# Optimization experiments

Measured on AMD Instinct MI355X. Metric: run time of the kernel, lower is better.

Reference implementation:

```python
import jax, jax.numpy as jnp
import numpy as np

N = 100000   # nodes
E = 1600000  # edges (avg degree 16)
D = 64       # channels (in = hidden = out)
L = 3        # layers


def setup_inputs() -> dict:
    key = jax.random.key(0)
    ks = jax.random.split(key, 8)
    s = 1.0 / np.sqrt(D)
    x = jax.random.normal(ks[0], (N, D), jnp.float32)
    edge_index = jax.random.randint(ks[1], (2, E), 0, N, dtype=jnp.int32)
    edge_type = jax.random.randint(ks[2], (E,), 0, 5, dtype=jnp.int32)
    Wq = jax.random.normal(ks[3], (L, D, D), jnp.float32) * s
    Wk = jax.random.normal(ks[4], (L, D, D), jnp.float32) * s
    Wv = jax.random.normal(ks[5], (L, D, D), jnp.float32) * s
    Ws = jax.random.normal(ks[6], (L, D, D), jnp.float32) * s
    bq = jnp.zeros((L, D), jnp.float32)
    bk = jnp.zeros((L, D), jnp.float32)
    bv = jnp.zeros((L, D), jnp.float32)
    bs = jnp.zeros((L, D), jnp.float32)
    return {"x": x, "edge_index": edge_index, "edge_type": edge_type,
            "Wq": Wq, "bq": bq, "Wk": Wk, "bk": bk,
            "Wv": Wv, "bv": bv, "Ws": Ws, "bs": bs}


def _transformer_conv(x, src, dst, Wq, bq, Wk, bk, Wv, bv, Ws, bs):
    # PyG TransformerConv, heads=1, concat=True, root_weight=True, beta=False
    q = x @ Wq + bq            # [N, D]
    k = x @ Wk + bk            # [N, D]
    v = x @ Wv + bv            # [N, D]
    scale = 1.0 / jnp.sqrt(jnp.asarray(D, x.dtype))
    # per-edge attention logits: <q_i, k_j> / sqrt(D)
    alpha = jnp.sum(q[dst] * k[src], axis=-1) * scale   # [E]
    # scatter-softmax over incoming edges of each target node
    m = jax.ops.segment_max(alpha, dst, num_segments=N)  # [N]
    e = jnp.exp(alpha - m[dst])                          # [E]
    denom = jax.ops.segment_sum(e, dst, num_segments=N)  # [N]
    a = e / (denom[dst] + 1e-16)                         # [E]
    # scatter-add aggregation of alpha * v_j
    agg = jax.ops.segment_sum(a[:, None] * v[src], dst, num_segments=N)  # [N, D]
    # root/skip connection (lin_skip with bias)
    return agg + x @ Ws + bs


def reference(x, edge_index, edge_type, Wq, bq, Wk, bk, Wv, bv, Ws, bs):
    src, dst = edge_index[0], edge_index[1]
    h = x
    for i in range(L):
        h = _transformer_conv(h, src, dst, Wq[i], bq[i], Wk[i], bk[i],
                              Wv[i], bv[i], Ws[i], bs[i])
        if i < L - 1:
            h = jax.nn.relu(h)
            # F.dropout(p=0.4) is identity in eval mode
    return h
```

## Files before the change

kernel.cpp:

```cpp
#include <hip/hip_runtime.h>

#define D 64
#define LAYERS 3
#define BSHIFT 8
#define NBMAX 512
#define CHUNK 4096
#define WSTRIDE 72

typedef unsigned short ushort_t;
typedef __bf16 bf16x8 __attribute__((ext_vector_type(8)));
typedef float f32x4 __attribute__((ext_vector_type(4)));

__device__ __forceinline__ ushort_t f2bf(float f) {
    unsigned b = __float_as_uint(f);
    b += 0x7FFFu + ((b >> 16) & 1u);
    return (ushort_t)(b >> 16);
}
__device__ __forceinline__ float bflo(unsigned u) { return __uint_as_float(u << 16); }
__device__ __forceinline__ float bfhi(unsigned u) { return __uint_as_float(u & 0xFFFF0000u); }

__global__ __launch_bounds__(256) void proj_kernel(
    const float* __restrict__ x,
    const float* __restrict__ Wq, const float* __restrict__ bq,
    const float* __restrict__ Wk, const float* __restrict__ bk,
    const float* __restrict__ Wv, const float* __restrict__ bv,
    const float* __restrict__ Ws, const float* __restrict__ bs,
    ushort_t* __restrict__ qb, ushort_t* __restrict__ kv,
    ushort_t* __restrict__ sk, int N)
{
    __shared__ ushort_t xs[32 * WSTRIDE];
    __shared__ ushort_t wt[4 * 64 * WSTRIDE];

    const int t = threadIdx.x;
    const int block_row = blockIdx.x * 32;

    {
        const int r  = t >> 3;
        const int c8 = (t & 7) * 8;
        const int row = block_row + r;
        float4 x0, x1;
        if (row < N) {
            x0 = *(const float4*)(x + (size_t)row * D + c8);
            x1 = *(const float4*)(x + (size_t)row * D + c8 + 4);
        } else {
            x0 = make_float4(0.f,0.f,0.f,0.f); x1 = x0;
        }
        uint4 u;
        u.x = (unsigned)f2bf(x0.x) | ((unsigned)f2bf(x0.y) << 16);
        u.y = (unsigned)f2bf(x0.z) | ((unsigned)f2bf(x0.w) << 16);
        u.z = (unsigned)f2bf(x1.x) | ((unsigned)f2bf(x1.y) << 16);
        u.w = (unsigned)f2bf(x1.z) | ((unsigned)f2bf(x1.w) << 16);
        *(uint4*)(xs + r * WSTRIDE + c8) = u;
    }
    {
        const float* Wm[4] = {Wq, Wk, Wv, Ws};
#pragma unroll
        for (int m = 0; m < 4; ++m) {
            const float* W = Wm[m];
            ushort_t* wtm = wt + m * 64 * WSTRIDE;
#pragma unroll
            for (int i = 0; i < 16; ++i) {
                const int e = i * 256 + t;
                const int k = e >> 6, n = e & 63;
                wtm[n * WSTRIDE + k] = f2bf(W[e]);
            }
        }
    }
    __syncthreads();

    const int l  = t & 63;
    const int w  = t >> 6;
    const int lr = l & 15;
    const int lk = (l >> 4) * 8;

    bf16x8 afr[2][2];
#pragma unroll
    for (int rt = 0; rt < 2; ++rt)
#pragma unroll
        for (int ks = 0; ks < 2; ++ks)
            afr[rt][ks] = *(const bf16x8*)(xs + (rt*16 + lr) * WSTRIDE + ks*32 + lk);

    const ushort_t* wtw = wt + w * 64 * WSTRIDE;
    f32x4 acc[2][4];
#pragma unroll
    for (int rt = 0; rt < 2; ++rt)
#pragma unroll
        for (int ct = 0; ct < 4; ++ct)
            acc[rt][ct] = (f32x4){0.f, 0.f, 0.f, 0.f};

#pragma unroll
    for (int ct = 0; ct < 4; ++ct) {
        const bf16x8 b0 = *(const bf16x8*)(wtw + (ct*16 + lr) * WSTRIDE + lk);
        const bf16x8 b1 = *(const bf16x8*)(wtw + (ct*16 + lr) * WSTRIDE + 32 + lk);
        acc[0][ct] = __builtin_amdgcn_mfma_f32_16x16x32_bf16(afr[0][0], b0, acc[0][ct], 0, 0, 0);
        acc[0][ct] = __builtin_amdgcn_mfma_f32_16x16x32_bf16(afr[0][1], b1, acc[0][ct], 0, 0, 0);
        acc[1][ct] = __builtin_amdgcn_mfma_f32_16x16x32_bf16(afr[1][0], b0, acc[1][ct], 0, 0, 0);
        acc[1][ct] = __builtin_amdgcn_mfma_f32_16x16x32_bf16(afr[1][1], b1, acc[1][ct], 0, 0, 0);
    }

    const float* biasW = (w == 0) ? bq : (w == 1) ? bk : (w == 2) ? bv : bs;
    float bcol[4];
#pragma unroll
    for (int ct = 0; ct < 4; ++ct) bcol[ct] = biasW[ct*16 + lr];

#pragma unroll
    for (int rt = 0; rt < 2; ++rt) {
#pragma unroll
        for (int ct = 0; ct < 4; ++ct) {
#pragma unroll
            for (int r = 0; r < 4; ++r) {
                const int row = block_row + rt*16 + (l >> 4) * 4 + r;
                const int col = ct*16 + lr;
                if (row < N) {
                    const float val = acc[rt][ct][r] + bcol[ct];
                    if (w == 0)      qb[(size_t)row * D + col] = f2bf(val);
                    else if (w == 3) sk[(size_t)row * D + col] = f2bf(val);
                    else {
                        ushort_t* kvr = kv + (size_t)row * 128;
                        kvr[(col >> 2) * 8 + ((w == 2) ? 4 : 0) + (col & 3)] = f2bf(val);
                    }
                }
            }
        }
    }
}

__global__ __launch_bounds__(256) void b_hist_kernel(
    const int* __restrict__ dst, int* __restrict__ bcount, int E)
{
    __shared__ int h[NBMAX];
    const int t = threadIdx.x;
    h[t] = 0; h[t + 256] = 0;
    __syncthreads();
    const int base = blockIdx.x * CHUNK;
#pragma unroll
    for (int i = 0; i < 16; ++i) {
        const int e = base + i * 256 + t;
        if (e < E) atomicAdd(h + (dst[e] >> BSHIFT), 1);
    }
    __syncthreads();
    if (h[t])       atomicAdd(bcount + t, h[t]);
    if (h[t + 256]) atomicAdd(bcount + t + 256, h[t + 256]);
}

__global__ __launch_bounds__(512) void b_scan_kernel(
    const int* __restrict__ bcount, int* __restrict__ bbase,
    int* __restrict__ gcursor, int E)
{
    __shared__ int tmp[NBMAX];
    const int t = threadIdx.x;
    const int val = bcount[t];
    tmp[t] = val;
    __syncthreads();
    for (int off = 1; off < NBMAX; off <<= 1) {
        int x = (t >= off) ? tmp[t - off] : 0;
        __syncthreads();
        tmp[t] += x;
        __syncthreads();
    }
    const int excl = tmp[t] - val;
    bbase[t] = excl;
    gcursor[t] = excl;
    if (t == NBMAX - 1) bbase[NBMAX] = E;
}

__global__ __launch_bounds__(256) void b_scatter_kernel(
    const int* __restrict__ src, const int* __restrict__ dst,
    int* __restrict__ gcursor, uint2* __restrict__ packed, int E)
{
    __shared__ int h[NBMAX];
    __shared__ int gb[NBMAX];
    const int t = threadIdx.x;
    h[t] = 0; h[t + 256] = 0;
    __syncthreads();

    const int base = blockIdx.x * CHUNK;
    int ls[16], ld[16], lr[16];
#pragma unroll
    for (int i = 0; i < 16; ++i) {
        const int e = base + i * 256 + t;
        if (e < E) {
            ls[i] = src[e];
            ld[i] = dst[e];
            lr[i] = atomicAdd(h + (ld[i] >> BSHIFT), 1);
        }
    }
    __syncthreads();
    for (int b = t; b < NBMAX; b += 256) {
        const int c = h[b];
        gb[b] = c ? atomicAdd(gcursor + b, c) : 0;
    }
    __syncthreads();
#pragma unroll
    for (int i = 0; i < 16; ++i) {
        const int e = base + i * 256 + t;
        if (e < E) {
            const int pos = gb[ld[i] >> BSHIFT] + lr[i];
            packed[pos] = make_uint2((unsigned)ls[i], (unsigned)ld[i]);
        }
    }
}

__global__ __launch_bounds__(256) void b_final_kernel(
    const uint2* __restrict__ packed, const int* __restrict__ bbase,
    int* __restrict__ esrc, int* __restrict__ offs, int* __restrict__ counts,
    int N)
{
    __shared__ int hist[256];
    __shared__ int scan[256];
    __shared__ int cursor[256];
    const int t = threadIdx.x;
    const int b = blockIdx.x;
    const int s = bbase[b];
    const int e = bbase[b + 1];

    hist[t] = 0;
    __syncthreads();
    for (int j = s + t; j < e; j += 256) {
        atomicAdd(hist + (packed[j].y & 255), 1);
    }
    __syncthreads();
    const int val = hist[t];
    scan[t] = val;
    __syncthreads();
    for (int off = 1; off < 256; off <<= 1) {
        int x = (t >= off) ? scan[t - off] : 0;
        __syncthreads();
        scan[t] += x;
        __syncthreads();
    }
    const int excl = scan[t] - val;
    const int node = b * 256 + t;
    if (node < N) {
        counts[node] = val;
        offs[node]   = s + excl;
    }
    cursor[t] = excl;
    __syncthreads();
    for (int j = s + t; j < e; j += 256) {
        const uint2 p = packed[j];
        const int r = atomicAdd(cursor + (p.y & 255), 1);
        esrc[s + r] = (int)p.x;
    }
}

__global__ __launch_bounds__(256) void node_kernel(
    const ushort_t* __restrict__ qb, const uint4* __restrict__ kv,
    const int* __restrict__ esrc, const int* __restrict__ offs,
    const int* __restrict__ counts, const ushort_t* __restrict__ sk,
    float* __restrict__ hout, int N, int do_relu)
{
    const int t = threadIdx.x;
    const int lane = t & 15;
    const int node = blockIdx.x * 16 + (t >> 4);
    if (node >= N) return;

    const int start = offs[node];
    const int end   = start + counts[node];

    const uint2 qu = *(const uint2*)(qb + (size_t)node * D + lane * 4);
    float4 qv;
    qv.x = bflo(qu.x); qv.y = bfhi(qu.x);
    qv.z = bflo(qu.y); qv.w = bfhi(qu.y);

    float m = -INFINITY, ssum = 0.0f;
    float4 acc = make_float4(0.0f, 0.0f, 0.0f, 0.0f);

    int j = start;
    for (; j + 2 <= end; j += 2) {
        const int s0 = esrc[j];
        const int s1 = esrc[j + 1];
        const uint4 u0 = kv[(size_t)s0 * 16 + lane];
        const uint4 u1 = kv[(size_t)s1 * 16 + lane];

        float p0 = bflo(u0.x) * qv.x + bfhi(u0.x) * qv.y
                 + bflo(u0.y) * qv.z + bfhi(u0.y) * qv.w;
        float p1 = bflo(u1.x) * qv.x + bfhi(u1.x) * qv.y
                 + bflo(u1.y) * qv.z + bfhi(u1.y) * qv.w;
        p0 += __shfl_xor(p0, 1);  p1 += __shfl_xor(p1, 1);
        p0 += __shfl_xor(p0, 2);  p1 += __shfl_xor(p1, 2);
        p0 += __shfl_xor(p0, 4);  p1 += __shfl_xor(p1, 4);
        p0 += __shfl_xor(p0, 8);  p1 += __shfl_xor(p1, 8);
        p0 *= 0.125f;  p1 *= 0.125f;

        const float mx = fmaxf(p0, p1);
        if (mx > m) {
            const float sc = __expf(m - mx);
            ssum *= sc;
            acc.x *= sc; acc.y *= sc; acc.z *= sc; acc.w *= sc;
            m = mx;
        }
        const float w0 = __expf(p0 - m);
        const float w1 = __expf(p1 - m);
        ssum += w0 + w1;
        acc.x = fmaf(w0, bflo(u0.z), fmaf(w1, bflo(u1.z), acc.x));
        acc.y = fmaf(w0, bfhi(u0.z), fmaf(w1, bfhi(u1.z), acc.y));
        acc.z = fmaf(w0, bflo(u0.w), fmaf(w1, bflo(u1.w), acc.z));
        acc.w = fmaf(w0, bfhi(u0.w), fmaf(w1, bfhi(u1.w), acc.w));
    }
    if (j < end) {
        const int s0 = esrc[j];
        const uint4 u0 = kv[(size_t)s0 * 16 + lane];
        float p0 = bflo(u0.x) * qv.x + bfhi(u0.x) * qv.y
                 + bflo(u0.y) * qv.z + bfhi(u0.y) * qv.w;
        p0 += __shfl_xor(p0, 1);
        p0 += __shfl_xor(p0, 2);
        p0 += __shfl_xor(p0, 4);
        p0 += __shfl_xor(p0, 8);
        p0 *= 0.125f;
        if (p0 > m) {
            const float sc = __expf(m - p0);
            ssum *= sc;
            acc.x *= sc; acc.y *= sc; acc.z *= sc; acc.w *= sc;
            m = p0;
        }
        const float w0 = __expf(p0 - m);
        ssum += w0;
        acc.x = fmaf(w0, bflo(u0.z), acc.x);
        acc.y = fmaf(w0, bfhi(u0.z), acc.y);
        acc.z = fmaf(w0, bflo(u0.w), acc.z);
        acc.w = fmaf(w0, bfhi(u0.w), acc.w);
    }

    const float inv = 1.0f / (ssum + 1e-16f);
    const uint2 su = *(const uint2*)(sk + (size_t)node * D + lane * 4);
    float4 ov;
    ov.x = fmaf(acc.x, inv, bflo(su.x));
    ov.y = fmaf(acc.y, inv, bfhi(su.x));
    ov.z = fmaf(acc.z, inv, bflo(su.y));
    ov.w = fmaf(acc.w, inv, bfhi(su.y));
    if (do_relu) {
        ov.x = fmaxf(ov.x, 0.0f); ov.y = fmaxf(ov.y, 0.0f);
        ov.z = fmaxf(ov.z, 0.0f); ov.w = fmaxf(ov.w, 0.0f);
    }
    *(float4*)(hout + (size_t)node * D + lane * 4) = ov;
}

extern "C" void kernel_launch(void* const* d_in, const int* in_sizes, int n_in,
                              void* d_out, int out_size, void* d_ws, size_t ws_size,
                              hipStream_t stream)
{
    const float* x   = (const float*)d_in[0];
    const int* ei    = (const int*)d_in[1];
    const float* Wq  = (const float*)d_in[3];
    const float* bq  = (const float*)d_in[4];
    const float* Wk  = (const float*)d_in[5];
    const float* bk  = (const float*)d_in[6];
    const float* Wv  = (const float*)d_in[7];
    const float* bv  = (const float*)d_in[8];
    const float* Ws  = (const float*)d_in[9];
    const float* bs  = (const float*)d_in[10];

    const int N = in_sizes[0] / D;
    const int E = in_sizes[2];
    const int* src = ei;
    const int* dst = ei + E;
    const int NB = (N + 255) / 256;

    ushort_t* qb = (ushort_t*)d_ws;
    ushort_t* kv = qb + (size_t)N * D;
    ushort_t* sk = kv + (size_t)N * 128;
    float* h0    = (float*)(sk + (size_t)N * D);
    float* h1    = h0 + (size_t)N * D;
    int* esrc    = (int*)(h1 + (size_t)N * D);
    uint2* packed = (uint2*)(esrc + E);
    int* counts  = (int*)(packed + E);
    int* offs    = counts + NBMAX * 256;
    int* bcount  = offs + NBMAX * 256;
    int* bbase   = bcount + NBMAX;
    int* gcursor = bbase + NBMAX + 1;

    hipMemsetAsync(bcount, 0, NBMAX * 4, stream);
    const int p1_blocks = (E + CHUNK - 1) / CHUNK;
    b_hist_kernel<<<p1_blocks, 256, 0, stream>>>(dst, bcount, E);
    b_scan_kernel<<<1, NBMAX, 0, stream>>>(bcount, bbase, gcursor, E);
    b_scatter_kernel<<<p1_blocks, 256, 0, stream>>>(src, dst, gcursor, packed, E);
    b_final_kernel<<<NB, 256, 0, stream>>>(packed, bbase, esrc, offs, counts, N);

    const int proj_blocks = (N + 31) / 32;
    const int node_blocks = (N + 15) / 16;

    const float* cur = x;
    for (int l = 0; l < LAYERS; ++l) {
        float* hout = (l == LAYERS - 1) ? (float*)d_out : (l & 1 ? h1 : h0);

        proj_kernel<<<proj_blocks, 256, 0, stream>>>(
            cur,
            Wq + (size_t)l * D * D, bq + (size_t)l * D,
            Wk + (size_t)l * D * D, bk + (size_t)l * D,
            Wv + (size_t)l * D * D, bv + (size_t)l * D,
            Ws + (size_t)l * D * D, bs + (size_t)l * D,
            qb, kv, sk, N);

        node_kernel<<<node_blocks, 256, 0, stream>>>(
            qb, (const uint4*)kv, esrc, offs, counts, sk, hout, N,
            l < LAYERS - 1 ? 1 : 0);

        cur = hout;
    }
}
```

Before: 359.6 us.

## Pre-convert weights and activations to bf16, drop LDS staging, pack edge keys

Weights are converted and transposed to bf16 once per call in a separate kernel, and the input is pre-converted to bf16. The projection kernel now reads MFMA fragments straight from global memory instead of staging x and all four weight matrices through shared memory with a barrier. Intermediate layer outputs are written as bf16, which halves activation traffic between layers. The edge-sort packed buffer shrinks from 8 to 4 bytes per edge by storing the low dst byte with src in one word, which assumes node indices fit in 24 bits and adds an extra launch for the conversions.

Measured after the change: 360.2 us. About the same (+0.2%).

```diff
diff --git a/kernel.cpp b/kernel.cpp
--- a/kernel.cpp
+++ b/kernel.cpp
@@ -5,7 +5,6 @@
 #define BSHIFT 8
 #define NBMAX 512
 #define CHUNK 4096
-#define WSTRIDE 72
 
 typedef unsigned short ushort_t;
 typedef __bf16 bf16x8 __attribute__((ext_vector_type(8)));
@@ -19,68 +18,68 @@
 __device__ __forceinline__ float bflo(unsigned u) { return __uint_as_float(u << 16); }
 __device__ __forceinline__ float bfhi(unsigned u) { return __uint_as_float(u & 0xFFFF0000u); }
 
+__global__ __launch_bounds__(256) void conv_x_kernel(
+    const float* __restrict__ x, ushort_t* __restrict__ xb, int n)
+{
+    const int g = blockIdx.x * 256 + threadIdx.x;
+    const int i = g * 8;
+    if (i >= n) return;
+    const float4 x0 = *(const float4*)(x + i);
+    const float4 x1 = *(const float4*)(x + i + 4);
+    uint4 u;
+    u.x = (unsigned)f2bf(x0.x) | ((unsigned)f2bf(x0.y) << 16);
+    u.y = (unsigned)f2bf(x0.z) | ((unsigned)f2bf(x0.w) << 16);
+    u.z = (unsigned)f2bf(x1.x) | ((unsigned)f2bf(x1.y) << 16);
+    u.w = (unsigned)f2bf(x1.z) | ((unsigned)f2bf(x1.w) << 16);
+    *(uint4*)(xb + i) = u;
+}
+
+__global__ __launch_bounds__(256) void conv_w_kernel(
+    const float* __restrict__ Wq, const float* __restrict__ Wk,
+    const float* __restrict__ Wv, const float* __restrict__ Ws,
+    ushort_t* __restrict__ wtb)
+{
+    const int b = blockIdx.x;
+    const int l = b >> 2, m = b & 3;
+    const float* W = ((m == 0) ? Wq : (m == 1) ? Wk : (m == 2) ? Wv : Ws)
+                     + (size_t)l * D * D;
+    ushort_t* out = wtb + (size_t)b * D * D;
+    const int t = threadIdx.x;
+#pragma unroll
+    for (int i = 0; i < 16; ++i) {
+        const int e = i * 256 + t;
+        const int n = e >> 6, k = e & 63;
+        out[n * D + k] = f2bf(W[k * D + n]);
+    }
+}
+
 __global__ __launch_bounds__(256) void proj_kernel(
-    const float* __restrict__ x,
-    const float* __restrict__ Wq, const float* __restrict__ bq,
-    const float* __restrict__ Wk, const float* __restrict__ bk,
-    const float* __restrict__ Wv, const float* __restrict__ bv,
-    const float* __restrict__ Ws, const float* __restrict__ bs,
+    const ushort_t* __restrict__ hb,
+    const ushort_t* __restrict__ wtb_l,
+    const float* __restrict__ bq, const float* __restrict__ bk,
+    const float* __restrict__ bv, const float* __restrict__ bs,
     ushort_t* __restrict__ qb, ushort_t* __restrict__ kv,
     ushort_t* __restrict__ sk, int N)
 {
-    __shared__ ushort_t xs[32 * WSTRIDE];
-    __shared__ ushort_t wt[4 * 64 * WSTRIDE];
-
     const int t = threadIdx.x;
     const int block_row = blockIdx.x * 32;
-
-    {
-        const int r  = t >> 3;
-        const int c8 = (t & 7) * 8;
-        const int row = block_row + r;
-        float4 x0, x1;
-        if (row < N) {
-            x0 = *(const float4*)(x + (size_t)row * D + c8);
-            x1 = *(const float4*)(x + (size_t)row * D + c8 + 4);
-        } else {
-            x0 = make_float4(0.f,0.f,0.f,0.f); x1 = x0;
-        }
-        uint4 u;
-        u.x = (unsigned)f2bf(x0.x) | ((unsigned)f2bf(x0.y) << 16);
-        u.y = (unsigned)f2bf(x0.z) | ((unsigned)f2bf(x0.w) << 16);
-        u.z = (unsigned)f2bf(x1.x) | ((unsigned)f2bf(x1.y) << 16);
-        u.w = (unsigned)f2bf(x1.z) | ((unsigned)f2bf(x1.w) << 16);
-        *(uint4*)(xs + r * WSTRIDE + c8) = u;
-    }
-    {
-        const float* Wm[4] = {Wq, Wk, Wv, Ws};
-#pragma unroll
-        for (int m = 0; m < 4; ++m) {
-            const float* W = Wm[m];
-            ushort_t* wtm = wt + m * 64 * WSTRIDE;
-#pragma unroll
-            for (int i = 0; i < 16; ++i) {
-                const int e = i * 256 + t;
-                const int k = e >> 6, n = e & 63;
-                wtm[n * WSTRIDE + k] = f2bf(W[e]);
-            }
-        }
-    }
-    __syncthreads();
-
     const int l  = t & 63;
     const int w  = t >> 6;
     const int lr = l & 15;
-    const int lk = (l >> 4) * 8;
+    const int hi = l >> 4;
+    const int lk = hi * 8;
 
     bf16x8 afr[2][2];
 #pragma unroll
-    for (int rt = 0; rt < 2; ++rt)
+    for (int rt = 0; rt < 2; ++rt) {
+        const int row = block_row + rt * 16 + lr;
+        const size_t base = (size_t)min(row, N - 1) * D;
 #pragma unroll
         for (int ks = 0; ks < 2; ++ks)
-            afr[rt][ks] = *(const bf16x8*)(xs + (rt*16 + lr) * WSTRIDE + ks*32 + lk);
-
-    const ushort_t* wtw = wt + w * 64 * WSTRIDE;
+            afr[rt][ks] = *(const bf16x8*)(hb + base + ks * 32 + lk);
+    }
+
+    const ushort_t* wtw = wtb_l + (size_t)w * D * D;
     f32x4 acc[2][4];
 #pragma unroll
     for (int rt = 0; rt < 2; ++rt)
@@ -90,8 +89,8 @@
 
 #pragma unroll
     for (int ct = 0; ct < 4; ++ct) {
-        const bf16x8 b0 = *(const bf16x8*)(wtw + (ct*16 + lr) * WSTRIDE + lk);
-        const bf16x8 b1 = *(const bf16x8*)(wtw + (ct*16 + lr) * WSTRIDE + 32 + lk);
+        const bf16x8 b0 = *(const bf16x8*)(wtw + (ct * 16 + lr) * D + lk);
+        const bf16x8 b1 = *(const bf16x8*)(wtw + (ct * 16 + lr) * D + 32 + lk);
         acc[0][ct] = __builtin_amdgcn_mfma_f32_16x16x32_bf16(afr[0][0], b0, acc[0][ct], 0, 0, 0);
         acc[0][ct] = __builtin_amdgcn_mfma_f32_16x16x32_bf16(afr[0][1], b1, acc[0][ct], 0, 0, 0);
         acc[1][ct] = __builtin_amdgcn_mfma_f32_16x16x32_bf16(afr[1][0], b0, acc[1][ct], 0, 0, 0);
@@ -101,7 +100,7 @@
     const float* biasW = (w == 0) ? bq : (w == 1) ? bk : (w == 2) ? bv : bs;
     float bcol[4];
 #pragma unroll
-    for (int ct = 0; ct < 4; ++ct) bcol[ct] = biasW[ct*16 + lr];
+    for (int ct = 0; ct < 4; ++ct) bcol[ct] = biasW[ct * 16 + lr];
 
 #pragma unroll
     for (int rt = 0; rt < 2; ++rt) {
@@ -109,8 +108,8 @@
         for (int ct = 0; ct < 4; ++ct) {
 #pragma unroll
             for (int r = 0; r < 4; ++r) {
-                const int row = block_row + rt*16 + (l >> 4) * 4 + r;
-                const int col = ct*16 + lr;
+                const int row = block_row + rt * 16 + hi * 4 + r;
+                const int col = ct * 16 + lr;
                 if (row < N) {
                     const float val = acc[rt][ct][r] + bcol[ct];
                     if (w == 0)      qb[(size_t)row * D + col] = f2bf(val);
@@ -166,7 +165,7 @@
 
 __global__ __launch_bounds__(256) void b_scatter_kernel(
     const int* __restrict__ src, const int* __restrict__ dst,
-    int* __restrict__ gcursor, uint2* __restrict__ packed, int E)
+    int* __restrict__ gcursor, unsigned* __restrict__ packed, int E)
 {
     __shared__ int h[NBMAX];
     __shared__ int gb[NBMAX];
@@ -196,13 +195,13 @@
         const int e = base + i * 256 + t;
         if (e < E) {
             const int pos = gb[ld[i] >> BSHIFT] + lr[i];
-            packed[pos] = make_uint2((unsigned)ls[i], (unsigned)ld[i]);
+            packed[pos] = ((unsigned)(ld[i] & 255) << 24) | (unsigned)ls[i];
         }
     }
 }
 
 __global__ __launch_bounds__(256) void b_final_kernel(
-    const uint2* __restrict__ packed, const int* __restrict__ bbase,
+    const unsigned* __restrict__ packed, const int* __restrict__ bbase,
     int* __restrict__ esrc, int* __restrict__ offs, int* __restrict__ counts,
     int N)
 {
@@ -217,7 +216,7 @@
     hist[t] = 0;
     __syncthreads();
     for (int j = s + t; j < e; j += 256) {
-        atomicAdd(hist + (packed[j].y & 255), 1);
+        atomicAdd(hist + (packed[j] >> 24), 1);
     }
     __syncthreads();
     const int val = hist[t];
@@ -238,9 +237,9 @@
     cursor[t] = excl;
     __syncthreads();
     for (int j = s + t; j < e; j += 256) {
-        const uint2 p = packed[j];
-        const int r = atomicAdd(cursor + (p.y & 255), 1);
-        esrc[s + r] = (int)p.x;
+        const unsigned p = packed[j];
+        const int r = atomicAdd(cursor + (p >> 24), 1);
+        esrc[s + r] = (int)(p & 0xFFFFFFu);
     }
 }
 
@@ -248,7 +247,8 @@
     const ushort_t* __restrict__ qb, const uint4* __restrict__ kv,
     const int* __restrict__ esrc, const int* __restrict__ offs,
     const int* __restrict__ counts, const ushort_t* __restrict__ sk,
-    float* __restrict__ hout, int N, int do_relu)
+    ushort_t* __restrict__ hb_out, float* __restrict__ hf_out,
+    int N, int mode)
 {
     const int t = threadIdx.x;
     const int lane = t & 15;
@@ -329,11 +329,16 @@
     ov.y = fmaf(acc.y, inv, bfhi(su.x));
     ov.z = fmaf(acc.z, inv, bflo(su.y));
     ov.w = fmaf(acc.w, inv, bfhi(su.y));
-    if (do_relu) {
+    if (mode == 0) {
         ov.x = fmaxf(ov.x, 0.0f); ov.y = fmaxf(ov.y, 0.0f);
         ov.z = fmaxf(ov.z, 0.0f); ov.w = fmaxf(ov.w, 0.0f);
-    }
-    *(float4*)(hout + (size_t)node * D + lane * 4) = ov;
+        uint2 u;
+        u.x = (unsigned)f2bf(ov.x) | ((unsigned)f2bf(ov.y) << 16);
+        u.y = (unsigned)f2bf(ov.z) | ((unsigned)f2bf(ov.w) << 16);
+        *(uint2*)(hb_out + (size_t)node * D + lane * 4) = u;
+    } else {
+        *(float4*)(hf_out + (size_t)node * D + lane * 4) = ov;
+    }
 }
 
 extern "C" void kernel_launch(void* const* d_in, const int* in_sizes, int n_in,
@@ -357,18 +362,23 @@
     const int* dst = ei + E;
     const int NB = (N + 255) / 256;
 
-    ushort_t* qb = (ushort_t*)d_ws;
-    ushort_t* kv = qb + (size_t)N * D;
-    ushort_t* sk = kv + (size_t)N * 128;
-    float* h0    = (float*)(sk + (size_t)N * D);
-    float* h1    = h0 + (size_t)N * D;
-    int* esrc    = (int*)(h1 + (size_t)N * D);
-    uint2* packed = (uint2*)(esrc + E);
+    ushort_t* xb  = (ushort_t*)d_ws;
+    ushort_t* hb0 = xb  + (size_t)N * D;
+    ushort_t* hb1 = hb0 + (size_t)N * D;
+    ushort_t* qb  = hb1 + (size_t)N * D;
+    ushort_t* sk  = qb  + (size_t)N * D;
+    ushort_t* kv  = sk  + (size_t)N * D;
+    ushort_t* wtb = kv  + (size_t)N * 128;
+    int* esrc     = (int*)(wtb + LAYERS * 4 * D * D);
+    unsigned* packed = (unsigned*)(esrc + E);
     int* counts  = (int*)(packed + E);
     int* offs    = counts + NBMAX * 256;
     int* bcount  = offs + NBMAX * 256;
     int* bbase   = bcount + NBMAX;
     int* gcursor = bbase + NBMAX + 1;
+
+    conv_x_kernel<<<(N * D + 2047) / 2048, 256, 0, stream>>>(x, xb, N * D);
+    conv_w_kernel<<<LAYERS * 4, 256, 0, stream>>>(Wq, Wk, Wv, Ws, wtb);
 
     hipMemsetAsync(bcount, 0, NBMAX * 4, stream);
     const int p1_blocks = (E + CHUNK - 1) / CHUNK;
@@ -380,22 +390,21 @@
     const int proj_blocks = (N + 31) / 32;
     const int node_blocks = (N + 15) / 16;
 
-    const float* cur = x;
+    const ushort_t* cur = xb;
     for (int l = 0; l < LAYERS; ++l) {
-        float* hout = (l == LAYERS - 1) ? (float*)d_out : (l & 1 ? h1 : h0);
+        const int last = (l == LAYERS - 1);
+        ushort_t* hb_out = (l & 1) ? hb1 : hb0;
 
         proj_kernel<<<proj_blocks, 256, 0, stream>>>(
-            cur,
-            Wq + (size_t)l * D * D, bq + (size_t)l * D,
-            Wk + (size_t)l * D * D, bk + (size_t)l * D,
-            Wv + (size_t)l * D * D, bv + (size_t)l * D,
-            Ws + (size_t)l * D * D, bs + (size_t)l * D,
+            cur, wtb + (size_t)l * 4 * D * D,
+            bq + (size_t)l * D, bk + (size_t)l * D,
+            bv + (size_t)l * D, bs + (size_t)l * D,
             qb, kv, sk, N);
 
         node_kernel<<<node_blocks, 256, 0, stream>>>(
-            qb, (const uint4*)kv, esrc, offs, counts, sk, hout, N,
-            l < LAYERS - 1 ? 1 : 0);
-
-        cur = hout;
-    }
-}
+            qb, (const uint4*)kv, esrc, offs, counts, sk,
+            hb_out, (float*)d_out, N, last ? 1 : 0);
+
+        cur = hb_out;
+    }
+}
```
